# Kernel optimization log

Measured on AMD Instinct MI355X. Metric: run time of the kernel, lower is better.

Reference implementation:

```python
import jax, jax.numpy as jnp
import numpy as np

N_NODES = 100000


def _gcn_layer(x, W, src, dst, w):
    # GCNConv(add_self_loops=False, normalize=False, bias=False):
    # h = x @ W; out[i] = sum_{e: dst[e]=i} w[e] * h[src[e]]
    h = x @ W                                   # [N, nhid]
    msgs = h[src] * w[:, None]                  # [E, nhid] gather + scale
    return jax.ops.segment_sum(msgs, dst, num_segments=N_NODES)  # scatter-add


def setup_inputs() -> dict:
    key = jax.random.key(0)
    ks = jax.random.split(key, 7)
    N, E, P, F, H = N_NODES, 1000000, 500000, 128, 64
    x = jax.random.normal(ks[0], (N, F), dtype=jnp.float32)
    edge_index = jax.random.randint(ks[1], (2, E), 0, N, dtype=jnp.int64)
    edge_weight = jax.random.uniform(ks[2], (E,), dtype=jnp.float32)
    pos_edge_index = jax.random.randint(ks[3], (2, P), 0, N, dtype=jnp.int64)
    W1 = jax.random.normal(ks[4], (F, H), dtype=jnp.float32) * (1.0 / np.sqrt(F))
    W2 = jax.random.normal(ks[5], (H, H), dtype=jnp.float32) * (1.0 / np.sqrt(H))
    Wlin = jax.random.normal(ks[6], (2, 2 * H), dtype=jnp.float32) * (1.0 / np.sqrt(2 * H))
    return {"x": x, "edge_index": edge_index, "edge_weight": edge_weight,
            "pos_edge_index": pos_edge_index, "W1": W1, "W2": W2, "Wlin": Wlin}


def reference(x, edge_index, edge_weight, pos_edge_index, W1, W2, Wlin):
    src, dst = edge_index[0], edge_index[1]
    h = jax.nn.relu(_gcn_layer(x, W1, src, dst, edge_weight))   # conv1 + relu
    z = _gcn_layer(h, W2, src, dst, edge_weight)                # conv2
    # decode: gather endpoint embeddings, concat, linear (no bias)
    pairs = jnp.concatenate([z[pos_edge_index[0]], z[pos_edge_index[1]]], axis=1)  # [P, 2H]
    return pairs @ Wlin.T                                       # [P, 2]
```

## Files before the change

### kernel.cpp

```cpp
#include <hip/hip_runtime.h>

#define F_IN 128
#define H_DIM 64
#define NBUCK_MAX 1024
#define BCAP 1664

typedef short s16x8 __attribute__((ext_vector_type(8)));
typedef float f32x4 __attribute__((ext_vector_type(4)));
typedef float f32x2 __attribute__((ext_vector_type(2)));

union FragU {
    s16x8 s;
    uint4 q;
    unsigned short u[8];
};

__device__ __forceinline__ unsigned short f2bf(float f) {
    unsigned int b = __float_as_uint(f);
    b += 0x7fffu + ((b >> 16) & 1u);
    return (unsigned short)(b >> 16);
}
__device__ __forceinline__ float bf2f(unsigned short u) {
    return __uint_as_float((unsigned int)u << 16);
}
__device__ __forceinline__ f32x2 up2(unsigned int v) {
    f32x2 r;
    r.x = __uint_as_float(v << 16);
    r.y = __uint_as_float(v & 0xffff0000u);
    return r;
}
__device__ __forceinline__ f32x2 fma2(f32x2 a, f32x2 b, f32x2 c) {
#if __has_builtin(__builtin_elementwise_fma)
    return __builtin_elementwise_fma(a, b, c);
#else
    f32x2 r;
    r.x = fmaf(a.x, b.x, c.x);
    r.y = fmaf(a.y, b.y, c.y);
    return r;
#endif
}

__device__ __forceinline__ void prepack_one(const float* __restrict__ W,
                                            unsigned short* __restrict__ wf, int KS, int tid) {
    int lane = tid & 63;
    int grp = tid >> 6;
    int ks = grp % KS;
    int ct = grp / KS;
    int col = ct * 16 + (lane & 15);
    int kbase = ks * 32 + (lane >> 4) * 8;
    FragU f;
#pragma unroll
    for (int j = 0; j < 8; ++j) f.u[j] = f2bf(W[(kbase + j) * H_DIM + col]);
    reinterpret_cast<uint4*>(wf)[tid] = f.q;
}

__global__ __launch_bounds__(256) void prepack_k(const float* __restrict__ W1, const float* __restrict__ W2,
                                                 unsigned short* __restrict__ wf1, unsigned short* __restrict__ wf2,
                                                 int* __restrict__ gcursor) {
    int tid = blockIdx.x * 256 + threadIdx.x;
    if (tid < NBUCK_MAX) gcursor[tid] = tid * BCAP;
    if (tid < 4 * 4 * 64) prepack_one(W1, wf1, 4, tid);
    else if (tid < 4 * 4 * 64 + 4 * 2 * 64) prepack_one(W2, wf2, 2, tid - 4 * 4 * 64);
}

__global__ __launch_bounds__(256) void gemm1_k(const float* __restrict__ x,
                                               const unsigned short* __restrict__ wf,
                                               unsigned short* __restrict__ outb, int N) {
    constexpr int KS = F_IN / 32;
    int wv = threadIdx.x >> 6;
    int lane = threadIdx.x & 63;
    int rb = blockIdx.x * 64 + wv * 16;
    int ra = rb + (lane & 15);
    if (ra > N - 1) ra = N - 1;
    int koct = lane >> 4;

    FragU af[KS];
    const float* ap = x + (size_t)ra * F_IN + koct * 8;
#pragma unroll
    for (int ks = 0; ks < KS; ++ks) {
        float4 v0 = *reinterpret_cast<const float4*>(ap + ks * 32);
        float4 v1 = *reinterpret_cast<const float4*>(ap + ks * 32 + 4);
        af[ks].u[0] = f2bf(v0.x); af[ks].u[1] = f2bf(v0.y);
        af[ks].u[2] = f2bf(v0.z); af[ks].u[3] = f2bf(v0.w);
        af[ks].u[4] = f2bf(v1.x); af[ks].u[5] = f2bf(v1.y);
        af[ks].u[6] = f2bf(v1.z); af[ks].u[7] = f2bf(v1.w);
    }

    const uint4* bq = reinterpret_cast<const uint4*>(wf);
    f32x4 acc[4];
#pragma unroll
    for (int ct = 0; ct < 4; ++ct) acc[ct] = (f32x4){0.f, 0.f, 0.f, 0.f};
#pragma unroll
    for (int ct = 0; ct < 4; ++ct) {
#pragma unroll
        for (int ks = 0; ks < KS; ++ks) {
            FragU b;
            b.q = bq[(ct * KS + ks) * 64 + lane];
            acc[ct] = __builtin_amdgcn_mfma_f32_16x16x32_bf16(af[ks].s, b.s, acc[ct], 0, 0, 0);
        }
    }

    int ro_base = rb + (lane >> 4) * 4;
    int col = lane & 15;
#pragma unroll
    for (int ct = 0; ct < 4; ++ct) {
#pragma unroll
        for (int j = 0; j < 4; ++j) {
            int ro = ro_base + j;
            if (ro < N) outb[(size_t)ro * H_DIM + ct * 16 + col] = f2bf(acc[ct][j]);
        }
    }
}

__global__ __launch_bounds__(256) void gemm2v_k(const unsigned short* __restrict__ a1b,
                                                const unsigned short* __restrict__ wf,
                                                const float* __restrict__ Wlin,
                                                float4* __restrict__ uz, int N) {
    constexpr int KS = H_DIM / 32;
    int wv = threadIdx.x >> 6;
    int lane = threadIdx.x & 63;
    int rb = blockIdx.x * 64 + wv * 16;
    int ra = rb + (lane & 15);
    if (ra > N - 1) ra = N - 1;
    int koct = lane >> 4;

    FragU af[KS];
    const unsigned short* ap = a1b + (size_t)ra * H_DIM + koct * 8;
#pragma unroll
    for (int ks = 0; ks < KS; ++ks)
        af[ks].q = *reinterpret_cast<const uint4*>(ap + ks * 32);

    const uint4* bq = reinterpret_cast<const uint4*>(wf);
    f32x4 acc[4];
#pragma unroll
    for (int ct = 0; ct < 4; ++ct) acc[ct] = (f32x4){0.f, 0.f, 0.f, 0.f};
#pragma unroll
    for (int ct = 0; ct < 4; ++ct) {
#pragma unroll
        for (int ks = 0; ks < KS; ++ks) {
            FragU b;
            b.q = bq[(ct * KS + ks) * 64 + lane];
            acc[ct] = __builtin_amdgcn_mfma_f32_16x16x32_bf16(af[ks].s, b.s, acc[ct], 0, 0, 0);
        }
    }

    int c = lane & 15;
    float w0[4], w1[4], w2[4], w3[4];
#pragma unroll
    for (int ct = 0; ct < 4; ++ct) {
        int col = ct * 16 + c;
        w0[ct] = Wlin[col];
        w1[ct] = Wlin[128 + col];
        w2[ct] = Wlin[64 + col];
        w3[ct] = Wlin[192 + col];
    }
    int ro_base = rb + (lane >> 4) * 4;
#pragma unroll
    for (int j = 0; j < 4; ++j) {
        float p0 = 0.f, p1 = 0.f, p2 = 0.f, p3 = 0.f;
#pragma unroll
        for (int ct = 0; ct < 4; ++ct) {
            float zv = acc[ct][j];
            p0 = fmaf(zv, w0[ct], p0);
            p1 = fmaf(zv, w1[ct], p1);
            p2 = fmaf(zv, w2[ct], p2);
            p3 = fmaf(zv, w3[ct], p3);
        }
#pragma unroll
        for (int m = 1; m < 16; m <<= 1) {
            p0 += __shfl_xor(p0, m);
            p1 += __shfl_xor(p1, m);
            p2 += __shfl_xor(p2, m);
            p3 += __shfl_xor(p3, m);
        }
        int ro = ro_base + j;
        if (c == 0 && ro < N) uz[ro] = make_float4(p0, p1, p2, p3);
    }
}

__global__ __launch_bounds__(256) void binA_k(const int* __restrict__ ei, const float* __restrict__ ew,
                                              int* __restrict__ gcursor,
                                              unsigned long long* __restrict__ stage, int E, int nbuck) {
    __shared__ unsigned long long sstage[4096];
    __shared__ int smeta[4096];
    __shared__ int cnt[NBUCK_MAX];
    __shared__ int lbase[NBUCK_MAX];
    __shared__ int gbase[NBUCK_MAX];
    __shared__ int cur[NBUCK_MAX];
    __shared__ int wsum[256];
    int tid = threadIdx.x;
    int e0 = blockIdx.x * 4096;
    int ecount = min(4096, E - e0);
    for (int i = tid; i < nbuck; i += 256) { cnt[i] = 0; cur[i] = 0; }
    __syncthreads();
    for (int i = tid; i < ecount; i += 256)
        atomicAdd(&cnt[ei[E + e0 + i] >> 7], 1);
    __syncthreads();
    int idx4 = tid * 4;
    int c[4];
    int mysum = 0;
#pragma unroll
    for (int j = 0; j < 4; ++j) {
        c[j] = (idx4 + j < nbuck) ? cnt[idx4 + j] : 0;
        mysum += c[j];
    }
    wsum[tid] = mysum;
    __syncthreads();
    for (int off = 1; off < 256; off <<= 1) {
        int add = (tid >= off) ? wsum[tid - off] : 0;
        __syncthreads();
        wsum[tid] += add;
        __syncthreads();
    }
    int run = wsum[tid] - mysum;
#pragma unroll
    for (int j = 0; j < 4; ++j) {
        if (idx4 + j < nbuck) lbase[idx4 + j] = run;
        run += c[j];
    }
    __syncthreads();
    for (int b = tid; b < nbuck; b += 256)
        gbase[b] = cnt[b] ? atomicAdd(&gcursor[b], cnt[b]) : 0;
    __syncthreads();
    for (int i = tid; i < ecount; i += 256) {
        int e = e0 + i;
        int s = ei[e];
        int d = ei[E + e];
        unsigned int wb = __float_as_uint(ew[e]);
        int b = d >> 7;
        int off = atomicAdd(&cur[b], 1);
        int pos = lbase[b] + off;
        sstage[pos] = ((unsigned long long)(d & 127) << 49)
                    | ((unsigned long long)(unsigned int)s << 32) | wb;
        smeta[pos] = gbase[b] + off;
    }
    __syncthreads();
    for (int i = tid; i < ecount; i += 256)
        stage[smeta[i]] = sstage[i];
}

__global__ __launch_bounds__(256) void binB_k(const unsigned long long* __restrict__ stage,
                                              const int* __restrict__ gcursor,
                                              unsigned long long* __restrict__ epack,
                                              int2* __restrict__ rdeg, int N) {
    __shared__ unsigned long long lout[2048];
    __shared__ int cnt[128], exc[128], cur[128];
    int b = blockIdx.x;
    int tid = threadIdx.x;
    int base = b * BCAP;
    int nb = gcursor[b] - base;
    if (tid < 128) { cnt[tid] = 0; cur[tid] = 0; }
    __syncthreads();
    for (int i = tid; i < nb; i += 256)
        atomicAdd(&cnt[(int)((stage[base + i] >> 49) & 127)], 1);
    __syncthreads();
    if (tid < 128) exc[tid] = cnt[tid];
    __syncthreads();
    for (int off = 1; off < 128; off <<= 1) {
        int add = (tid >= off && tid < 128) ? exc[tid - off] : 0;
        __syncthreads();
        if (tid < 128) exc[tid] += add;
        __syncthreads();
    }
    int node0 = b * 128;
    if (tid < 128) {
        exc[tid] -= cnt[tid];
        int node = node0 + tid;
        if (node < N) rdeg[node] = make_int2(base + exc[tid], cnt[tid]);
    }
    __syncthreads();
    for (int i = tid; i < nb; i += 256) {
        unsigned long long v = stage[base + i];
        int dl = (int)((v >> 49) & 127);
        unsigned int src = (unsigned int)((v >> 32) & 0x1FFFF);
        unsigned int wb = (unsigned int)v;
        int pos = exc[dl] + atomicAdd(&cur[dl], 1);
        lout[pos] = ((unsigned long long)wb << 32) | src;
    }
    __syncthreads();
    for (int i = tid; i < nb; i += 256)
        epack[base + i] = lout[i];
}

__global__ __launch_bounds__(256) void agg1_k(const unsigned short* __restrict__ hb,
                                              const int2* __restrict__ rdeg,
                                              const unsigned long long* __restrict__ epack,
                                              unsigned short* __restrict__ outb, int N) {
    int wid = (blockIdx.x * 256 + threadIdx.x) >> 6;
    int lane = threadIdx.x & 63;
    int ng = lane >> 2;
    int dimg = lane & 3;
    int node = wid * 16 + ng;
    if (node >= N) return;
    int2 rd = rdeg[node];
    int start = rd.x, cnt = rd.y;
    f32x2 acc[8];
#pragma unroll
    for (int q = 0; q < 8; ++q) acc[q] = (f32x2){0.f, 0.f};
    const uint4* hbase = reinterpret_cast<const uint4*>(hb);
    for (int j = 0; j < cnt; ++j) {
        unsigned long long p = epack[start + j];
        float w = __uint_as_float((unsigned int)(p >> 32));
        f32x2 w2 = {w, w};
        unsigned int src = (unsigned int)p;
        const uint4* rp = hbase + (size_t)src * (H_DIM / 8) + dimg * 2;
        uint4 v0 = rp[0];
        uint4 v1 = rp[1];
        acc[0] = fma2(w2, up2(v0.x), acc[0]);
        acc[1] = fma2(w2, up2(v0.y), acc[1]);
        acc[2] = fma2(w2, up2(v0.z), acc[2]);
        acc[3] = fma2(w2, up2(v0.w), acc[3]);
        acc[4] = fma2(w2, up2(v1.x), acc[4]);
        acc[5] = fma2(w2, up2(v1.y), acc[5]);
        acc[6] = fma2(w2, up2(v1.z), acc[6]);
        acc[7] = fma2(w2, up2(v1.w), acc[7]);
    }
    unsigned int pk[8];
#pragma unroll
    for (int q = 0; q < 8; ++q)
        pk[q] = (unsigned int)f2bf(fmaxf(acc[q].x, 0.f))
              | ((unsigned int)f2bf(fmaxf(acc[q].y, 0.f)) << 16);
    uint4* op = reinterpret_cast<uint4*>(outb + (size_t)node * H_DIM + dimg * 16);
    op[0] = make_uint4(pk[0], pk[1], pk[2], pk[3]);
    op[1] = make_uint4(pk[4], pk[5], pk[6], pk[7]);
}

__global__ __launch_bounds__(256) void aggv_k(const float4* __restrict__ uz,
                                              const int2* __restrict__ rdeg,
                                              const unsigned long long* __restrict__ epack,
                                              float4* __restrict__ u, int N) {
    int node = blockIdx.x * 256 + threadIdx.x;
    if (node >= N) return;
    int2 rd = rdeg[node];
    int start = rd.x, cnt = rd.y;
    float4 acc = make_float4(0.f, 0.f, 0.f, 0.f);
    int j = 0;
    for (; j + 3 < cnt; j += 4) {
#pragma unroll
        for (int q = 0; q < 4; ++q) {
            unsigned long long p = epack[start + j + q];
            float w = __uint_as_float((unsigned int)(p >> 32));
            float4 v = uz[(unsigned int)p];
            acc.x = fmaf(w, v.x, acc.x);
            acc.y = fmaf(w, v.y, acc.y);
            acc.z = fmaf(w, v.z, acc.z);
            acc.w = fmaf(w, v.w, acc.w);
        }
    }
    for (; j < cnt; ++j) {
        unsigned long long p = epack[start + j];
        float w = __uint_as_float((unsigned int)(p >> 32));
        float4 v = uz[(unsigned int)p];
        acc.x = fmaf(w, v.x, acc.x);
        acc.y = fmaf(w, v.y, acc.y);
        acc.z = fmaf(w, v.z, acc.z);
        acc.w = fmaf(w, v.w, acc.w);
    }
    u[node] = acc;
}

__global__ __launch_bounds__(256) void pair_k(const float4* __restrict__ u,
                                              const int* __restrict__ pos,
                                              float2* __restrict__ out, int P) {
    int p = blockIdx.x * 256 + threadIdx.x;
    if (p >= P) return;
    int s = pos[p];
    int t = pos[P + p];
    float4 us = u[s];
    float4 ut = u[t];
    union { float f[2]; unsigned long long v; } o;
    o.f[0] = us.x + ut.z;
    o.f[1] = us.y + ut.w;
    __builtin_nontemporal_store(o.v, reinterpret_cast<unsigned long long*>(&out[p]));
}

extern "C" void kernel_launch(void* const* d_in, const int* in_sizes, int n_in,
                              void* d_out, int out_size, void* d_ws, size_t ws_size,
                              hipStream_t stream) {
    const float* x    = (const float*)d_in[0];
    const int*   ei   = (const int*)d_in[1];
    const float* ew   = (const float*)d_in[2];
    const int*   pos  = (const int*)d_in[3];
    const float* W1   = (const float*)d_in[4];
    const float* W2   = (const float*)d_in[5];
    const float* Wlin = (const float*)d_in[6];
    float* out = (float*)d_out;

    const int N = in_sizes[0] / F_IN;
    const int E = in_sizes[2];
    const int P = in_sizes[3] / 2;
    const int nbuck = (N + 127) / 128;

    char* ws = (char*)d_ws;
    const size_t rowBF = (size_t)N * H_DIM * sizeof(unsigned short);
    const size_t regionBytes = (size_t)nbuck * BCAP * 8;
    unsigned short* hb   = (unsigned short*)ws;
    unsigned short* a1b  = (unsigned short*)(ws + rowBF);
    float4*         uz   = (float4*)(ws + 2 * rowBF);
    float4*         u    = uz + N;
    unsigned long long* stage = (unsigned long long*)((char*)(u + N));
    unsigned long long* epack = (unsigned long long*)((char*)stage + regionBytes);
    int* gcursor = (int*)((char*)epack + regionBytes);
    int2* rdeg   = (int2*)(gcursor + NBUCK_MAX);
    size_t wf_off = (((size_t)((char*)(rdeg + N) - ws)) + 15) & ~(size_t)15;
    unsigned short* wf1 = (unsigned short*)(ws + wf_off);
    unsigned short* wf2 = wf1 + 4 * 4 * 64 * 8;

    prepack_k<<<6, 256, 0, stream>>>(W1, W2, wf1, wf2, gcursor);

    gemm1_k<<<(N + 63) / 64, 256, 0, stream>>>(x, wf1, hb, N);

    binA_k<<<(E + 4095) / 4096, 256, 0, stream>>>(ei, ew, gcursor, stage, E, nbuck);
    binB_k<<<nbuck, 256, 0, stream>>>(stage, gcursor, epack, rdeg, N);

    agg1_k<<<(N + 63) / 64, 256, 0, stream>>>(hb, rdeg, epack, a1b, N);
    gemm2v_k<<<(N + 63) / 64, 256, 0, stream>>>(a1b, wf2, Wlin, uz, N);
    aggv_k<<<(N + 255) / 256, 256, 0, stream>>>(uz, rdeg, epack, u, N);
    pair_k<<<(P + 255) / 256, 256, 0, stream>>>(u, pos, (float2*)out, P);
}
```

Measured before the change: 99.28 us.

## Fuse bucket sort with first-layer aggregation using shared-memory edge lists

```diff
diff --git a/kernel.cpp b/kernel.cpp
--- a/kernel.cpp
+++ b/kernel.cpp
@@ -19,9 +19,6 @@
     unsigned int b = __float_as_uint(f);
     b += 0x7fffu + ((b >> 16) & 1u);
     return (unsigned short)(b >> 16);
-}
-__device__ __forceinline__ float bf2f(unsigned short u) {
-    return __uint_as_float((unsigned int)u << 16);
 }
 __device__ __forceinline__ f32x2 up2(unsigned int v) {
     f32x2 r;
@@ -239,11 +236,13 @@
         stage[smeta[i]] = sstage[i];
 }
 
-__global__ __launch_bounds__(256) void binB_k(const unsigned long long* __restrict__ stage,
-                                              const int* __restrict__ gcursor,
-                                              unsigned long long* __restrict__ epack,
-                                              int2* __restrict__ rdeg, int N) {
-    __shared__ unsigned long long lout[2048];
+__global__ __launch_bounds__(512) void aggsort1_k(const unsigned short* __restrict__ hb,
+                                                  const int* __restrict__ gcursor,
+                                                  const unsigned long long* __restrict__ stage,
+                                                  unsigned long long* __restrict__ epack,
+                                                  int2* __restrict__ rdeg,
+                                                  unsigned short* __restrict__ outb, int N) {
+    __shared__ unsigned long long lout[BCAP];
     __shared__ int cnt[128], exc[128], cur[128];
     int b = blockIdx.x;
     int tid = threadIdx.x;
@@ -251,7 +250,7 @@
     int nb = gcursor[b] - base;
     if (tid < 128) { cnt[tid] = 0; cur[tid] = 0; }
     __syncthreads();
-    for (int i = tid; i < nb; i += 256)
+    for (int i = tid; i < nb; i += 512)
         atomicAdd(&cnt[(int)((stage[base + i] >> 49) & 127)], 1);
     __syncthreads();
     if (tid < 128) exc[tid] = cnt[tid];
@@ -262,14 +261,13 @@
         if (tid < 128) exc[tid] += add;
         __syncthreads();
     }
-    int node0 = b * 128;
     if (tid < 128) {
         exc[tid] -= cnt[tid];
-        int node = node0 + tid;
+        int node = b * 128 + tid;
         if (node < N) rdeg[node] = make_int2(base + exc[tid], cnt[tid]);
     }
     __syncthreads();
-    for (int i = tid; i < nb; i += 256) {
+    for (int i = tid; i < nb; i += 512) {
         unsigned long long v = stage[base + i];
         int dl = (int)((v >> 49) & 127);
         unsigned int src = (unsigned int)((v >> 32) & 0x1FFFF);
@@ -278,42 +276,65 @@
         lout[pos] = ((unsigned long long)wb << 32) | src;
     }
     __syncthreads();
-    for (int i = tid; i < nb; i += 256)
+    for (int i = tid; i < nb; i += 512)
         epack[base + i] = lout[i];
-}
-
-__global__ __launch_bounds__(256) void agg1_k(const unsigned short* __restrict__ hb,
-                                              const int2* __restrict__ rdeg,
-                                              const unsigned long long* __restrict__ epack,
-                                              unsigned short* __restrict__ outb, int N) {
-    int wid = (blockIdx.x * 256 + threadIdx.x) >> 6;
-    int lane = threadIdx.x & 63;
-    int ng = lane >> 2;
-    int dimg = lane & 3;
-    int node = wid * 16 + ng;
+
+    int g = tid >> 2;
+    int dimg = tid & 3;
+    int node = b * 128 + g;
     if (node >= N) return;
-    int2 rd = rdeg[node];
-    int start = rd.x, cnt = rd.y;
+    int start = exc[g];
+    int cg = cnt[g];
     f32x2 acc[8];
 #pragma unroll
     for (int q = 0; q < 8; ++q) acc[q] = (f32x2){0.f, 0.f};
     const uint4* hbase = reinterpret_cast<const uint4*>(hb);
-    for (int j = 0; j < cnt; ++j) {
-        unsigned long long p = epack[start + j];
-        float w = __uint_as_float((unsigned int)(p >> 32));
-        f32x2 w2 = {w, w};
-        unsigned int src = (unsigned int)p;
-        const uint4* rp = hbase + (size_t)src * (H_DIM / 8) + dimg * 2;
-        uint4 v0 = rp[0];
-        uint4 v1 = rp[1];
-        acc[0] = fma2(w2, up2(v0.x), acc[0]);
-        acc[1] = fma2(w2, up2(v0.y), acc[1]);
-        acc[2] = fma2(w2, up2(v0.z), acc[2]);
-        acc[3] = fma2(w2, up2(v0.w), acc[3]);
-        acc[4] = fma2(w2, up2(v1.x), acc[4]);
-        acc[5] = fma2(w2, up2(v1.y), acc[5]);
-        acc[6] = fma2(w2, up2(v1.z), acc[6]);
-        acc[7] = fma2(w2, up2(v1.w), acc[7]);
+    int j = 0;
+    for (; j + 1 < cg; j += 2) {
+        unsigned long long p0 = lout[start + j];
+        unsigned long long p1 = lout[start + j + 1];
+        float wa = __uint_as_float((unsigned int)(p0 >> 32));
+        float wbv = __uint_as_float((unsigned int)(p1 >> 32));
+        f32x2 w2a = {wa, wa};
+        f32x2 w2b = {wbv, wbv};
+        const uint4* rp0 = hbase + (size_t)(unsigned int)p0 * (H_DIM / 8) + dimg * 2;
+        const uint4* rp1 = hbase + (size_t)(unsigned int)p1 * (H_DIM / 8) + dimg * 2;
+        uint4 a0 = rp0[0];
+        uint4 a1 = rp0[1];
+        uint4 b0 = rp1[0];
+        uint4 b1 = rp1[1];
+        acc[0] = fma2(w2a, up2(a0.x), acc[0]);
+        acc[1] = fma2(w2a, up2(a0.y), acc[1]);
+        acc[2] = fma2(w2a, up2(a0.z), acc[2]);
+        acc[3] = fma2(w2a, up2(a0.w), acc[3]);
+        acc[4] = fma2(w2a, up2(a1.x), acc[4]);
+        acc[5] = fma2(w2a, up2(a1.y), acc[5]);
+        acc[6] = fma2(w2a, up2(a1.z), acc[6]);
+        acc[7] = fma2(w2a, up2(a1.w), acc[7]);
+        acc[0] = fma2(w2b, up2(b0.x), acc[0]);
+        acc[1] = fma2(w2b, up2(b0.y), acc[1]);
+        acc[2] = fma2(w2b, up2(b0.z), acc[2]);
+        acc[3] = fma2(w2b, up2(b0.w), acc[3]);
+        acc[4] = fma2(w2b, up2(b1.x), acc[4]);
+        acc[5] = fma2(w2b, up2(b1.y), acc[5]);
+        acc[6] = fma2(w2b, up2(b1.z), acc[6]);
+        acc[7] = fma2(w2b, up2(b1.w), acc[7]);
+    }
+    if (j < cg) {
+        unsigned long long p0 = lout[start + j];
+        float wa = __uint_as_float((unsigned int)(p0 >> 32));
+        f32x2 w2a = {wa, wa};
+        const uint4* rp0 = hbase + (size_t)(unsigned int)p0 * (H_DIM / 8) + dimg * 2;
+        uint4 a0 = rp0[0];
+        uint4 a1 = rp0[1];
+        acc[0] = fma2(w2a, up2(a0.x), acc[0]);
+        acc[1] = fma2(w2a, up2(a0.y), acc[1]);
+        acc[2] = fma2(w2a, up2(a0.z), acc[2]);
+        acc[3] = fma2(w2a, up2(a0.w), acc[3]);
+        acc[4] = fma2(w2a, up2(a1.x), acc[4]);
+        acc[5] = fma2(w2a, up2(a1.y), acc[5]);
+        acc[6] = fma2(w2a, up2(a1.z), acc[6]);
+        acc[7] = fma2(w2a, up2(a1.w), acc[7]);
     }
     unsigned int pk[8];
 #pragma unroll
@@ -411,9 +432,8 @@
     gemm1_k<<<(N + 63) / 64, 256, 0, stream>>>(x, wf1, hb, N);
 
     binA_k<<<(E + 4095) / 4096, 256, 0, stream>>>(ei, ew, gcursor, stage, E, nbuck);
-    binB_k<<<nbuck, 256, 0, stream>>>(stage, gcursor, epack, rdeg, N);
-
-    agg1_k<<<(N + 63) / 64, 256, 0, stream>>>(hb, rdeg, epack, a1b, N);
+
+    aggsort1_k<<<nbuck, 512, 0, stream>>>(hb, gcursor, stage, epack, rdeg, a1b, N);
     gemm2v_k<<<(N + 63) / 64, 256, 0, stream>>>(a1b, wf2, Wlin, uz, N);
     aggv_k<<<(N + 255) / 256, 256, 0, stream>>>(uz, rdeg, epack, u, N);
     pair_k<<<(P + 255) / 256, 256, 0, stream>>>(u, pos, (float2*)out, P);
```

After: 92.85 us. 6.5% less time.
